# Kernel optimization log

Measured on AMD Instinct MI355X. Metric: run time of the kernel, lower is better.

## Reference

```python
import jax, jax.numpy as jnp
import numpy as np
from jax import lax

LN_EPS = 1e-5
GRN_EPS = 1e-6


def _convnext_block(x, cw, cb, lng, lnb, w1, b1, gg, gb, w2, b2):
    # x: [B, C, H, W] NCHW; cw: [C, 1, 7, 7] depthwise kernel
    dim = x.shape[1]
    y = lax.conv_general_dilated(
        x, cw, window_strides=(1, 1), padding=[(3, 3), (3, 3)],
        dimension_numbers=('NCHW', 'OIHW', 'NCHW'), feature_group_count=dim)
    y = y + cb[None, :, None, None]
    y = y.transpose(0, 2, 3, 1)  # NHWC
    # LayerNorm over channels
    mu = y.mean(-1, keepdims=True)
    var = ((y - mu) ** 2).mean(-1, keepdims=True)
    y = (y - mu) * lax.rsqrt(var + LN_EPS) * lng + lnb
    # pointwise expand
    y = y @ w1 + b1
    y = jax.nn.gelu(y, approximate=False)
    # Global Response Normalization
    gx = jnp.sqrt(jnp.sum(y * y, axis=(1, 2), keepdims=True))  # [B,1,1,C']
    nx = gx / (gx.mean(-1, keepdims=True) + GRN_EPS)
    y = gg * (y * nx) + gb + y
    # pointwise project
    y = y @ w2 + b2
    return y.transpose(0, 3, 1, 2) + x


def _stack_blocks(x, cw, cb, lng, lnb, w1, b1, gg, gb, w2, b2):
    for i in range(cw.shape[0]):
        x = _convnext_block(x, cw[i], cb[i], lng[i], lnb[i], w1[i], b1[i],
                            gg[i], gb[i], w2[i], b2[i])
    return x


def setup_inputs() -> dict:
    key = jax.random.key(0)
    B, C, H, W = 8, 256, 64, 64
    K = 1024
    INTER = 4 * C
    DEPTH = 2
    ks = jax.random.split(key, 8)
    x = jax.random.normal(ks[0], (B, C, H, W), jnp.float32)
    codebook = jax.random.uniform(ks[1], (K, C), jnp.float32, -1.0 / K, 1.0 / K)

    def make_params(k):
        k1, k2, k3 = jax.random.split(k, 3)
        return dict(
            conv_w=0.02 * jax.random.normal(k1, (DEPTH, C, 1, 7, 7), jnp.float32),
            conv_b=jnp.zeros((DEPTH, C), jnp.float32),
            ln_g=jnp.ones((DEPTH, C), jnp.float32),
            ln_b=jnp.zeros((DEPTH, C), jnp.float32),
            fc1_w=0.02 * jax.random.normal(k2, (DEPTH, C, INTER), jnp.float32),
            fc1_b=jnp.zeros((DEPTH, INTER), jnp.float32),
            grn_g=jnp.zeros((DEPTH, INTER), jnp.float32),
            grn_b=jnp.zeros((DEPTH, INTER), jnp.float32),
            fc2_w=0.02 * jax.random.normal(k3, (DEPTH, INTER, C), jnp.float32),
            fc2_b=jnp.zeros((DEPTH, C), jnp.float32),
        )

    enc = make_params(ks[2])
    dec = make_params(ks[3])
    out = {'x': x, 'codebook': codebook}
    for name, p in (('enc', enc), ('dec', dec)):
        for k2, v in p.items():
            out[f'{name}_{k2}'] = v
    return out


def reference(x, codebook,
              enc_conv_w, enc_conv_b, enc_ln_g, enc_ln_b, enc_fc1_w, enc_fc1_b,
              enc_grn_g, enc_grn_b, enc_fc2_w, enc_fc2_b,
              dec_conv_w, dec_conv_b, dec_ln_g, dec_ln_b, dec_fc1_w, dec_fc1_b,
              dec_grn_g, dec_grn_b, dec_fc2_w, dec_fc2_b):
    B, C, H, W = x.shape
    inputs = _stack_blocks(x, enc_conv_w, enc_conv_b, enc_ln_g, enc_ln_b,
                           enc_fc1_w, enc_fc1_b, enc_grn_g, enc_grn_b,
                           enc_fc2_w, enc_fc2_b)
    inputs = inputs.transpose(0, 2, 3, 1)  # [B,H,W,C]
    flat = inputs.reshape(-1, C)  # [N, C]
    # squared Euclidean distances (argmin invariant to sqrt)
    d2 = (jnp.sum(flat * flat, axis=1, keepdims=True)
          - 2.0 * (flat @ codebook.T)
          + jnp.sum(codebook * codebook, axis=1)[None, :])  # [N, K]
    encoding_indices = jnp.argmin(d2, axis=1)  # [N]
    quantized = codebook[encoding_indices].reshape(inputs.shape)  # [B,H,W,C]
    matched_indices = encoding_indices.reshape(B, H, W)
    # straight-through estimator
    quantized = lax.stop_gradient(quantized) + inputs - lax.stop_gradient(inputs)
    quantized = quantized.transpose(0, 3, 1, 2)  # [B,C,H,W]
    decoded = _stack_blocks(quantized, dec_conv_w, dec_conv_b, dec_ln_g, dec_ln_b,
                            dec_fc1_w, dec_fc1_b, dec_grn_g, dec_grn_b,
                            dec_fc2_w, dec_fc2_b)
    return quantized, decoded, matched_indices
```

## Files before the change

### kernel.cpp

```cpp
#include <hip/hip_runtime.h>
#include <math.h>
#include <stdint.h>

typedef unsigned short u16;
typedef unsigned long long u64;
typedef __attribute__((ext_vector_type(8))) short bf16x8;
typedef __attribute__((ext_vector_type(4))) float f32x4;

__device__ __forceinline__ u16 bfhi(float v) {
  unsigned u = __float_as_uint(v);
  u += 0x7FFFu + ((u >> 16) & 1u);
  return (u16)(u >> 16);
}
__device__ __forceinline__ float b2f(u16 h) { return __uint_as_float((unsigned)h << 16); }

__device__ __forceinline__ void gload16(void* lds, const void* g) {
  __builtin_amdgcn_global_load_lds(
      (const __attribute__((address_space(1))) unsigned int*)g,
      (__attribute__((address_space(3))) unsigned int*)lds, 16, 0, 0);
}

__global__ __launch_bounds__(256) void k_conv(const float* __restrict__ in,
                                              const float* __restrict__ cw,
                                              const float* __restrict__ cb,
                                              float* __restrict__ out) {
  const int bx = blockIdx.x;
  const int c = bx & 255;
  __shared__ float patch[70 * 76];
  const int t = threadIdx.x;
  const float* plane = in + (size_t)bx * 4096;
  for (int i = t; i < 1330; i += 256) {
    const int row = i / 19, cf = i - row * 19;
    const int bit = (row >> 2) & 1;
    const int gf = cf - 1 - bit;
    const int h = row - 3;
    float4 v = {0.f, 0.f, 0.f, 0.f};
    if ((unsigned)h < 64u && (unsigned)gf < 16u) v = *(const float4*)(plane + h * 64 + gf * 4);
    *(float4*)(patch + row * 76 + cf * 4) = v;
  }
  const float* wp = cw + c * 49;
  float wt[49];
#pragma unroll
  for (int i = 0; i < 49; ++i) wt[i] = wp[i];
  const float bias = cb[c];
  __syncthreads();
  const int j = t & 7, i = t >> 3;
  const int w0 = j * 8, h0 = i * 2;
  float acc[2][8];
#pragma unroll
  for (int dr = 0; dr < 2; ++dr)
#pragma unroll
    for (int ww = 0; ww < 8; ++ww) acc[dr][ww] = bias;
#pragma unroll
  for (int r = 0; r < 8; ++r) {
    const int prow = h0 + r;
    const int bit = (prow >> 2) & 1;
    const float* base = patch + prow * 76 + w0 + 4 * bit;
    float win[16];
#pragma unroll
    for (int q = 0; q < 4; ++q) {
      const float4 v = *(const float4*)(base + q * 4);
      win[q * 4 + 0] = v.x; win[q * 4 + 1] = v.y;
      win[q * 4 + 2] = v.z; win[q * 4 + 3] = v.w;
    }
#pragma unroll
    for (int dr = 0; dr < 2; ++dr) {
      const int kh = r - dr;
      if (kh >= 0 && kh < 7) {
#pragma unroll
        for (int kw = 0; kw < 7; ++kw) {
          const float wv = wt[kh * 7 + kw];
#pragma unroll
          for (int ww = 0; ww < 8; ++ww)
            acc[dr][ww] = fmaf(win[ww + kw + 1], wv, acc[dr][ww]);
        }
      }
    }
  }
  float* op = out + (size_t)bx * 4096;
#pragma unroll
  for (int dr = 0; dr < 2; ++dr) {
    const int hh = h0 + dr;
    float4 o1, o2;
    o1.x = acc[dr][0]; o1.y = acc[dr][1]; o1.z = acc[dr][2]; o1.w = acc[dr][3];
    o2.x = acc[dr][4]; o2.y = acc[dr][5]; o2.z = acc[dr][6]; o2.w = acc[dr][7];
    *(float4*)(op + hh * 64 + w0) = o1;
    *(float4*)(op + hh * 64 + w0 + 4) = o2;
  }
}

__global__ __launch_bounds__(256) void k_lnT(const float* __restrict__ src,
                                             const float* __restrict__ g,
                                             const float* __restrict__ bt,
                                             u16* __restrict__ Rh, u16* __restrict__ Rl,
                                             const int wlo) {
  __shared__ float T[256 * 33];
  __shared__ float red[8 * 32];
  __shared__ float gs[256], bs[256];
  const int t = threadIdx.x;
  const int n0 = blockIdx.x * 32;
  const int b = n0 >> 12, pl = n0 & 4095;
  gs[t] = g[t];
  bs[t] = bt[t];
  const int m = t & 7, h = t >> 3;
  const float* sp = src + (((size_t)(b * 256)) << 12) + pl + m * 4;
#pragma unroll
  for (int it = 0; it < 8; ++it) {
    const int c = it * 32 + h;
    const float4 v = *(const float4*)(sp + ((size_t)c << 12));
    *(float4*)(T + c * 33 + m * 4) = v;
  }
  __syncthreads();
  const int p = t & 31, qq = t >> 5;
  float s = 0.f;
#pragma unroll
  for (int jj = 0; jj < 32; ++jj) s += T[(qq * 32 + jj) * 33 + p];
  red[qq * 32 + p] = s;
  __syncthreads();
  float tot = 0.f;
#pragma unroll
  for (int k = 0; k < 8; ++k) tot += red[k * 32 + p];
  const float mu = tot * (1.0f / 256.0f);
  __syncthreads();
  float s2 = 0.f;
#pragma unroll
  for (int jj = 0; jj < 32; ++jj) {
    const float d = T[(qq * 32 + jj) * 33 + p] - mu;
    s2 = fmaf(d, d, s2);
  }
  red[qq * 32 + p] = s2;
  __syncthreads();
  float tot2 = 0.f;
#pragma unroll
  for (int k = 0; k < 8; ++k) tot2 += red[k * 32 + p];
  const float rs = 1.0f / sqrtf(tot2 * (1.0f / 256.0f) + 1e-5f);
#pragma unroll
  for (int jj = 0; jj < 32; ++jj) {
    const int c = qq * 32 + jj;
    const float y = (T[c * 33 + p] - mu) * rs * gs[c] + bs[c];
    const u16 hh = bfhi(y);
    const u16 ll = bfhi(y - b2f(hh));
    ((unsigned*)T)[c * 33 + p] = ((unsigned)hh << 16) | ll;
  }
  __syncthreads();
  const int w = t >> 6, l = t & 63;
  const unsigned* Tu = (const unsigned*)T;
#pragma unroll
  for (int r = 0; r < 4; ++r) {
    const int px = r * 8 + w * 2 + (l >> 5);
    const int c0 = (l & 31) * 8;
    unsigned hp[4], lp[4];
#pragma unroll
    for (int jj = 0; jj < 4; ++jj) {
      const unsigned a = Tu[(c0 + 2 * jj) * 33 + px];
      const unsigned bb = Tu[(c0 + 2 * jj + 1) * 33 + px];
      hp[jj] = (a >> 16) | (bb & 0xffff0000u);
      lp[jj] = (a & 0xffffu) | (bb << 16);
    }
    const size_t base = (size_t)(n0 + px) * 256 + c0;
    *(uint4*)(Rh + base) = make_uint4(hp[0], hp[1], hp[2], hp[3]);
    if (wlo) *(uint4*)(Rl + base) = make_uint4(lp[0], lp[1], lp[2], lp[3]);
  }
}

template <int KD, int SPLIT, int EPI, int NCT>
__global__ __launch_bounds__(256) void k_gemm(
    const u16* __restrict__ Ah_, const u16* __restrict__ Al_,
    const u16* __restrict__ Bh_, const u16* __restrict__ Bl_,
    const int row0, const long long bstride,
    const float* __restrict__ pbias,
    u16* __restrict__ poh, u16* __restrict__ pol,
    float* __restrict__ pxout, const float* __restrict__ pxin,
    float* __restrict__ pgx2, u64* __restrict__ pmin) {
  constexpr int BUF_B = (SPLIT ? 4 : 2) * 8192;
  constexpr int NBUF = SPLIT ? 1 : 2;
  constexpr int STAGE_B = NBUF * BUF_B;
  constexpr int TRANS_B = (EPI == 1) ? 64 * 129 * 4 : 0;
  constexpr int SMEM_B = STAGE_B > TRANS_B ? STAGE_B : TRANS_B;
  constexpr int NS = KD / 32;
  __shared__ __align__(16) char smem[SMEM_B];

  const int t = threadIdx.x;
  const int w = t >> 6, l = t & 63;
  const int quad = l >> 4, lm = l & 15;
  const int wr = (w & 1) * 64, wc = (w >> 1) * 64;
  const int id = blockIdx.x + gridDim.x * blockIdx.y;
  constexpr int L = (NCT == 8) ? 3 : 1;
  const int colt = (id >> 3) & (NCT - 1);
  const int rowt = (id & 7) + ((id >> (3 + L)) << 3);
  const int nblk0 = rowt * 128;
  const int bglob = (row0 + nblk0) >> 12;

  const u16* Agh = Ah_ + (size_t)nblk0 * KD;
  const u16* Agl = SPLIT ? (Al_ + (size_t)nblk0 * KD) : Ah_;
  const u16* Bgh = Bh_ + (size_t)bglob * (size_t)bstride + (size_t)(colt * 128) * KD;
  const u16* Bgl = SPLIT ? (Bl_ + (size_t)bglob * (size_t)bstride + (size_t)(colt * 128) * KD) : Bh_;

  f32x4 acc[4][4];
  const f32x4 zz = {0.f, 0.f, 0.f, 0.f};
#pragma unroll
  for (int i = 0; i < 4; ++i)
#pragma unroll
    for (int j = 0; j < 4; ++j) acc[i][j] = zz;

  auto stage32 = [&](char* Sp, const u16* Gp, int ks) {
#pragma unroll
    for (int ii = 0; ii < 2; ++ii) {
      const int o = ii * 4096 + t * 16;
      const int row = o >> 6;
      const int lc = ((o >> 4) & 3) ^ ((row >> 1) & 3);
      gload16(Sp + o, Gp + (size_t)row * KD + ks * 32 + lc * 8);
    }
  };
  auto stage_all = [&](int b, int ks) {
    char* base = smem + (size_t)b * BUF_B;
    stage32(base, Agh, ks);
    stage32(base + 8192, Bgh, ks);
    if constexpr (SPLIT) {
      stage32(base + 16384, Agl, ks);
      stage32(base + 24576, Bgl, ks);
    }
  };
  auto frag_at = [&](const u16* S, int rc) -> bf16x8 {
    const int sw = ((rc >> 1) & 3) ^ quad;
    return *(const bf16x8*)(S + rc * 32 + (sw << 3));
  };

  if constexpr (SPLIT) {
#pragma unroll 1
    for (int ks = 0; ks < NS; ++ks) {
      if (ks) __syncthreads();
      stage_all(0, ks);
      __syncthreads();
      const u16* base = (const u16*)smem;
      bf16x8 ah[4], bh[4], al[4], bl[4];
#pragma unroll
      for (int i = 0; i < 4; ++i) {
        ah[i] = frag_at(base, wr + i * 16 + lm);
        bh[i] = frag_at(base + 4096, wc + i * 16 + lm);
      }
#pragma unroll
      for (int i = 0; i < 4; ++i) {
        al[i] = frag_at(base + 8192, wr + i * 16 + lm);
        bl[i] = frag_at(base + 12288, wc + i * 16 + lm);
      }
#pragma unroll
      for (int i = 0; i < 4; ++i)
#pragma unroll
        for (int j = 0; j < 4; ++j)
          acc[i][j] = __builtin_amdgcn_mfma_f32_16x16x32_bf16(ah[i], bh[j], acc[i][j], 0, 0, 0);
#pragma unroll
      for (int i = 0; i < 4; ++i)
#pragma unroll
        for (int j = 0; j < 4; ++j)
          acc[i][j] = __builtin_amdgcn_mfma_f32_16x16x32_bf16(al[i], bh[j], acc[i][j], 0, 0, 0);
#pragma unroll
      for (int i = 0; i < 4; ++i)
#pragma unroll
        for (int j = 0; j < 4; ++j)
          acc[i][j] = __builtin_amdgcn_mfma_f32_16x16x32_bf16(ah[i], bl[j], acc[i][j], 0, 0, 0);
    }
  } else {
    stage_all(0, 0);
    __syncthreads();
#pragma unroll 1
    for (int ks = 0; ks < NS; ++ks) {
      const u16* base = (const u16*)(smem + (size_t)(ks & 1) * BUF_B);
      bf16x8 ah[4], bh[4];
#pragma unroll
      for (int i = 0; i < 4; ++i) {
        ah[i] = frag_at(base, wr + i * 16 + lm);
        bh[i] = frag_at(base + 4096, wc + i * 16 + lm);
      }
      if (ks + 1 < NS) stage_all((ks + 1) & 1, ks + 1);
      __builtin_amdgcn_sched_barrier(0);
#pragma unroll
      for (int i = 0; i < 4; ++i)
#pragma unroll
        for (int j = 0; j < 4; ++j)
          acc[i][j] = __builtin_amdgcn_mfma_f32_16x16x32_bf16(ah[i], bh[j], acc[i][j], 0, 0, 0);
      __syncthreads();
    }
  }

  if constexpr (EPI == 0) {
    float csum[4] = {0.f, 0.f, 0.f, 0.f};
    float bv[4];
#pragma unroll
    for (int j = 0; j < 4; ++j) bv[j] = pbias[colt * 128 + wc + j * 16 + lm];
#pragma unroll
    for (int i = 0; i < 4; ++i) {
#pragma unroll
      for (int r = 0; r < 4; ++r) {
        const int row = nblk0 + wr + i * 16 + quad * 4 + r;
#pragma unroll
        for (int j = 0; j < 4; ++j) {
          const int col = colt * 128 + wc + j * 16 + lm;
          const float x = acc[i][j][r] + bv[j];
          const float gl = 0.5f * x * (1.0f + erff(x * 0.70710678118654752f));
          csum[j] = fmaf(gl, gl, csum[j]);
          const size_t idx = (size_t)row * 1024 + col;
          const u16 h = bfhi(gl);
          poh[idx] = h;
          if constexpr (SPLIT) pol[idx] = bfhi(gl - b2f(h));
        }
      }
    }
#pragma unroll
    for (int j = 0; j < 4; ++j) {
      float cs = csum[j];
      cs += __shfl_xor(cs, 16);
      cs += __shfl_xor(cs, 32);
      if (quad == 0)
        unsafeAtomicAdd(&pgx2[bglob * 1024 + colt * 128 + wc + j * 16 + lm], cs);
    }
  } else if constexpr (EPI == 1) {
    float* T = (float*)smem;
    const int pg0 = (row0 + nblk0) & 4095;
    const int bb = (row0 + nblk0) >> 12;
#pragma unroll 1
    for (int h = 0; h < 2; ++h) {
      __syncthreads();
      if ((w >> 1) == h) {
#pragma unroll
        for (int i = 0; i < 4; ++i) {
          const int row = wr + i * 16 + quad * 4;
#pragma unroll
          for (int j = 0; j < 4; ++j) {
            const int cl = j * 16 + lm;
#pragma unroll
            for (int r = 0; r < 4; ++r) T[cl * 129 + row + r] = acc[i][j][r];
          }
        }
      }
      __syncthreads();
      const int lp = (l & 31) * 4;
      const int ch2 = l >> 5;
#pragma unroll
      for (int step = 0; step < 8; ++step) {
        const int cl = w * 16 + step * 2 + ch2;
        const int cg = colt * 128 + h * 64 + cl;
        float4 tv = *(float4*)&T[cl * 129 + lp];
        const float bv2 = pbias[cg];
        const size_t nchw = (((size_t)(bb * 256 + cg)) << 12) + pg0 + lp;
        const float4 xv = *(const float4*)(pxin + nchw);
        float4 z;
        z.x = tv.x + bv2 + xv.x;
        z.y = tv.y + bv2 + xv.y;
        z.z = tv.z + bv2 + xv.z;
        z.w = tv.w + bv2 + xv.w;
        if (pxout) *(float4*)(pxout + nchw) = z;
        if (poh) *(float4*)&T[cl * 129 + lp] = z;
      }
      if (poh) {
        __syncthreads();
        const int cl3 = t & 63;
        const int cg3 = colt * 128 + h * 64 + cl3;
        const int r0 = (t >> 6) * 32;
#pragma unroll
        for (int n = 0; n < 32; ++n) {
          const float z = T[cl3 * 129 + r0 + n];
          const size_t idx = (size_t)(nblk0 + r0 + n) * 256 + cg3;
          const u16 hh = bfhi(z);
          poh[idx] = hh;
          pol[idx] = bfhi(z - b2f(hh));
        }
      }
    }
  } else {
#pragma unroll
    for (int i = 0; i < 4; ++i) {
#pragma unroll
      for (int r = 0; r < 4; ++r) {
        const int nloc = nblk0 + wr + i * 16 + quad * 4 + r;
        const float tnv = pxin[nloc];
        u64 best = ~0ULL;
#pragma unroll
        for (int j = 0; j < 4; ++j) {
          const int code = colt * 128 + wc + j * 16 + lm;
          const float d = __fadd_rn(__fsub_rn(tnv, __fmul_rn(2.0f, acc[i][j][r])), pbias[code]);
          const u64 pk = (((u64)__float_as_uint(d)) << 32) | (unsigned)code;
          best = pk < best ? pk : best;
        }
#pragma unroll
        for (int off = 1; off < 16; off <<= 1) {
          unsigned lo32 = (unsigned)best, hi32 = (unsigned)(best >> 32);
          lo32 = __shfl_xor(lo32, off);
          hi32 = __shfl_xor(hi32, off);
          const u64 o2 = (((u64)hi32) << 32) | lo32;
          best = o2 < best ? o2 : best;
        }
        if (lm == 0) atomicMin(pmin + nloc, best);
      }
    }
  }
}

__global__ __launch_bounds__(256) void k_rownorm(const u16* __restrict__ Eh,
                                                 const u16* __restrict__ El,
                                                 float* __restrict__ tn) {
  const int t = threadIdx.x;
  const int r = t >> 2, p = t & 3;
  const int n = blockIdx.x * 64 + r;
  const u16* ph = Eh + (size_t)n * 256 + p * 64;
  const u16* pl = El + (size_t)n * 256 + p * 64;
  float s = 0.f;
#pragma unroll
  for (int j = 0; j < 8; ++j) {
    const uint4 hv = *(const uint4*)(ph + j * 8);
    const uint4 lv = *(const uint4*)(pl + j * 8);
    const unsigned hu[4] = {hv.x, hv.y, hv.z, hv.w};
    const unsigned lu[4] = {lv.x, lv.y, lv.z, lv.w};
#pragma unroll
    for (int q = 0; q < 4; ++q) {
      const float v0 = b2f((u16)(hu[q] & 0xffff)) + b2f((u16)(lu[q] & 0xffff));
      const float v1 = b2f((u16)(hu[q] >> 16)) + b2f((u16)(lu[q] >> 16));
      s = fmaf(v0, v0, s);
      s = fmaf(v1, v1, s);
    }
  }
  s += __shfl_xor(s, 1);
  s += __shfl_xor(s, 2);
  if (p == 0) tn[n] = s;
}

__global__ __launch_bounds__(256) void k_grn_scale(const float* __restrict__ GX2,
                                                   const float* __restrict__ gg,
                                                   float* __restrict__ S, int b0) {
  const int b = b0 + blockIdx.x, t = threadIdx.x;
  const float* gxb = GX2 + (size_t)b * 1024;
  float gx[4];
  float s = 0.f;
#pragma unroll
  for (int i = 0; i < 4; ++i) {
    gx[i] = sqrtf(gxb[t + i * 256]);
    s += gx[i];
  }
  const int w = t >> 6, l = t & 63;
#pragma unroll
  for (int o = 32; o > 0; o >>= 1) s += __shfl_down(s, o);
  __shared__ float red[4];
  __shared__ float bc;
  if (l == 0) red[w] = s;
  __syncthreads();
  if (t == 0) bc = 1.0f / ((red[0] + red[1] + red[2] + red[3]) * (1.0f / 1024.0f) + 1e-6f);
  __syncthreads();
  const float inv = bc;
#pragma unroll
  for (int i = 0; i < 4; ++i)
    S[(size_t)b * 1024 + t + i * 256] = fmaf(gg[t + i * 256], gx[i] * inv, 1.0f);
}

__global__ __launch_bounds__(256) void k_w2prep(const float* __restrict__ W2,
                                                const float* __restrict__ S, int b0,
                                                u16* __restrict__ Wh, u16* __restrict__ Wl) {
  const int bx = blockIdx.x;
  const int b = b0 + (bx >> 8), n = bx & 255;
  const int t = threadIdx.x;
#pragma unroll
  for (int j = 0; j < 4; ++j) {
    const int k = t + j * 256;
    const float v = W2[(size_t)k * 256 + n] * S[(size_t)b * 1024 + k];
    const size_t idx = ((size_t)(b * 256 + n)) * 1024 + k;
    const u16 h = bfhi(v);
    Wh[idx] = h;
    Wl[idx] = bfhi(v - b2f(h));
  }
}

__global__ __launch_bounds__(256) void k_bias2(const float* __restrict__ W2,
                                               const float* __restrict__ gb,
                                               const float* __restrict__ b2,
                                               float* __restrict__ out) {
  const int c = blockIdx.x, t = threadIdx.x;
  float acc = 0.f;
#pragma unroll
  for (int j = 0; j < 4; ++j) {
    const int k = t + j * 256;
    acc = fmaf(gb[k], W2[(size_t)k * 256 + c], acc);
  }
  const int w = t >> 6, l = t & 63;
#pragma unroll
  for (int o = 32; o > 0; o >>= 1) acc += __shfl_down(acc, o);
  __shared__ float red[4];
  if (l == 0) red[w] = acc;
  __syncthreads();
  if (t == 0) out[c] = red[0] + red[1] + red[2] + red[3] + b2[c];
}

__global__ __launch_bounds__(256) void k_wt(const float* __restrict__ W1,
                                            u16* __restrict__ Wh, u16* __restrict__ Wl) {
  const int bx = blockIdx.x;
  const int d = bx >> 10, n = bx & 1023;
  const int k = threadIdx.x;
  const float v = W1[(size_t)d * 262144 + (size_t)k * 1024 + n];
  const size_t idx = (size_t)bx * 256 + k;
  const u16 h = bfhi(v);
  Wh[idx] = h;
  Wl[idx] = bfhi(v - b2f(h));
}

__global__ __launch_bounds__(256) void k_csplit(const float* __restrict__ C,
                                                u16* __restrict__ Ch, u16* __restrict__ Cl) {
  const size_t i = (size_t)blockIdx.x * 256 + threadIdx.x;
  const float v = C[i];
  const u16 h = bfhi(v);
  Ch[i] = h;
  Cl[i] = bfhi(v - b2f(h));
}

__device__ __forceinline__ float np_pairwise_sq_256(const float* p) {
  float half[2];
#pragma unroll
  for (int hh = 0; hh < 2; ++hh) {
    float r[8];
#pragma unroll
    for (int j = 0; j < 8; ++j) {
      const float v = p[hh * 128 + j];
      r[j] = __fmul_rn(v, v);
    }
    for (int i = 8; i < 128; i += 8) {
#pragma unroll
      for (int j = 0; j < 8; ++j) {
        const float v = p[hh * 128 + i + j];
        r[j] = __fadd_rn(r[j], __fmul_rn(v, v));
      }
    }
    half[hh] = __fadd_rn(__fadd_rn(__fadd_rn(r[0], r[1]), __fadd_rn(r[2], r[3])),
                         __fadd_rn(__fadd_rn(r[4], r[5]), __fadd_rn(r[6], r[7])));
  }
  return __fadd_rn(half[0], half[1]);
}

__global__ __launch_bounds__(256) void k_c2(const float* __restrict__ cbk, float* __restrict__ c2) {
  const int k = blockIdx.x * 256 + threadIdx.x;
  c2[k] = np_pairwise_sq_256(cbk + (size_t)k * 256);
}

__global__ __launch_bounds__(256) void k_idx(const u64* __restrict__ pk, float* __restrict__ outI) {
  const int n = blockIdx.x * 256 + threadIdx.x;
  outI[n] = (float)(unsigned)(pk[n] & 0xffffffffULL);
}

__global__ __launch_bounds__(256) void k_gather(const u64* __restrict__ pk,
                                                const float* __restrict__ cbk,
                                                float* __restrict__ outq) {
  const int t = threadIdx.x;
  const int p0 = blockIdx.x * 64;
  const int b = p0 >> 12, pl = (p0 & 4095) + (t & 63);
  const int cg = t >> 6;
  const int n = p0 + (t & 63);
  const int k = (int)(unsigned)(pk[n] & 0xffffffffULL);
  const float* crow = cbk + (size_t)k * 256 + cg * 64;
  float* ob = outq + (((size_t)(b * 256 + cg * 64)) << 12) + pl;
#pragma unroll 1
  for (int j = 0; j < 16; ++j) {
    const float4 cv = *(const float4*)(crow + j * 4);
    ob[((size_t)(j * 4 + 0)) << 12] = cv.x;
    ob[((size_t)(j * 4 + 1)) << 12] = cv.y;
    ob[((size_t)(j * 4 + 2)) << 12] = cv.z;
    ob[((size_t)(j * 4 + 3)) << 12] = cv.w;
  }
}

extern "C" void kernel_launch(void* const* d_in, const int* in_sizes, int n_in,
                              void* d_out, int out_size, void* d_ws, size_t ws_size,
                              hipStream_t stream) {
  const float* x = (const float*)d_in[0];
  const float* cbk = (const float*)d_in[1];
  const float* Pe[10];
  const float* Pd[10];
  for (int i = 0; i < 10; ++i) Pe[i] = (const float*)d_in[2 + i];
  for (int i = 0; i < 10; ++i) Pd[i] = (const float*)d_in[12 + i];

  float* ws = (float*)d_ws;
  size_t o = 0;
  auto alloc = [&](size_t nf) {
    float* p = ws + o;
    o += (nf + 63) & ~(size_t)63;
    return p;
  };
  float* P1 = alloc(8388608);
  u16* Rh = (u16*)alloc(4194304);
  u16* Rl = (u16*)alloc(4194304);
  u16* W1th_e = (u16*)alloc(262144);
  u16* W1tl_e = (u16*)alloc(262144);
  u16* W1th_d = (u16*)alloc(262144);
  u16* W1tl_d = (u16*)alloc(262144);
  u16* W2sh = (u16*)alloc(1048576);
  u16* W2sl = (u16*)alloc(1048576);
  u16* Ch = (u16*)alloc(131072);
  u16* Cl = (u16*)alloc(131072);
  float* C2v = alloc(1024);
  float* GX2 = alloc(8192);
  float* Sv = alloc(8192);
  float* bias2v = alloc(256);
  float* tn = alloc(32768);
  u64* pk = (u64*)alloc(65536);
  const size_t fixedf = o;
  const size_t availf = (ws_size / 4 > fixedf) ? ws_size / 4 - fixedf : 0;
  int chunkB = (int)(availf / 4194304);
  if (chunkB > 8) chunkB = 8;
  if (chunkB < 1) chunkB = 1;
  float* Cv = ws + o;
  u16* Mh = (u16*)(ws + o);
  u16* Ml = (u16*)(ws + o + (size_t)chunkB * 2097152);

  float* outQ = (float*)d_out;
  float* outD = outQ + 8388608;
  float* outI = outD + 8388608;

  auto run_enc = [&](const float* xin, float* xout, u16* Eh, u16* El,
                     const float* const* pp, int d) {
    k_conv<<<2048, 256, 0, stream>>>(xin, pp[0] + (size_t)d * 256 * 49, pp[1] + d * 256, Cv);
    k_lnT<<<1024, 256, 0, stream>>>(Cv, pp[2] + d * 256, pp[3] + d * 256, Rh, Rl, 1);
    k_bias2<<<256, 256, 0, stream>>>(pp[8] + (size_t)d * 262144, pp[7] + d * 1024,
                                     pp[9] + d * 256, bias2v);
    hipMemsetAsync(GX2, 0, 8192 * 4, stream);
    for (int b0 = 0; b0 < 8; b0 += chunkB) {
      const int nb = (8 - b0 < chunkB) ? 8 - b0 : chunkB;
      k_gemm<256, 1, 0, 8><<<dim3(8, nb * 32), 256, 0, stream>>>(
          Rh + (size_t)b0 * 4096 * 256, Rl + (size_t)b0 * 4096 * 256,
          W1th_e + (size_t)d * 262144, W1tl_e + (size_t)d * 262144,
          b0 * 4096, 0, Pe[5] + d * 1024, Mh, Ml, nullptr, nullptr, GX2, nullptr);
      k_grn_scale<<<nb, 256, 0, stream>>>(GX2, pp[6] + d * 1024, Sv, b0);
      k_w2prep<<<nb * 256, 256, 0, stream>>>(pp[8] + (size_t)d * 262144, Sv, b0, W2sh, W2sl);
      k_gemm<1024, 1, 1, 2><<<dim3(2, nb * 32), 256, 0, stream>>>(
          Mh, Ml, W2sh, W2sl, b0 * 4096, 262144LL, bias2v,
          Eh ? Eh + (size_t)b0 * 4096 * 256 : (u16*)nullptr,
          El ? El + (size_t)b0 * 4096 * 256 : (u16*)nullptr,
          xout, xin, nullptr, nullptr);
    }
  };

  auto run_dec = [&](const float* xin, float* xout, const float* const* pp, int d) {
    k_conv<<<2048, 256, 0, stream>>>(xin, pp[0] + (size_t)d * 256 * 49, pp[1] + d * 256, Cv);
    k_lnT<<<1024, 256, 0, stream>>>(Cv, pp[2] + d * 256, pp[3] + d * 256, Rh, Rl, 0);
    k_bias2<<<256, 256, 0, stream>>>(pp[8] + (size_t)d * 262144, pp[7] + d * 1024,
                                     pp[9] + d * 256, bias2v);
    hipMemsetAsync(GX2, 0, 8192 * 4, stream);
    for (int b0 = 0; b0 < 8; b0 += chunkB) {
      const int nb = (8 - b0 < chunkB) ? 8 - b0 : chunkB;
      k_gemm<256, 0, 0, 8><<<dim3(8, nb * 32), 256, 0, stream>>>(
          Rh + (size_t)b0 * 4096 * 256, nullptr,
          W1th_d + (size_t)d * 262144, nullptr,
          b0 * 4096, 0, Pd[5] + d * 1024, Mh, nullptr, nullptr, nullptr, GX2, nullptr);
      k_grn_scale<<<nb, 256, 0, stream>>>(GX2, pp[6] + d * 1024, Sv, b0);
      k_w2prep<<<nb * 256, 256, 0, stream>>>(pp[8] + (size_t)d * 262144, Sv, b0, W2sh, W2sl);
      k_gemm<1024, 0, 1, 2><<<dim3(2, nb * 32), 256, 0, stream>>>(
          Mh, nullptr, W2sh, nullptr, b0 * 4096, 262144LL, bias2v,
          nullptr, nullptr, xout, xin, nullptr, nullptr);
    }
  };

  k_wt<<<2048, 256, 0, stream>>>(Pe[4], W1th_e, W1tl_e);
  k_wt<<<2048, 256, 0, stream>>>(Pd[4], W1th_d, W1tl_d);
  k_csplit<<<1024, 256, 0, stream>>>(cbk, Ch, Cl);
  k_c2<<<4, 256, 0, stream>>>(cbk, C2v);

  run_enc(x, P1, nullptr, nullptr, Pe, 0);
  run_enc(P1, nullptr, Rh, Rl, Pe, 1);

  k_rownorm<<<512, 256, 0, stream>>>(Rh, Rl, tn);
  hipMemsetAsync(pk, 0xFF, 32768 * 8, stream);
  k_gemm<256, 1, 2, 8><<<dim3(8, 256), 256, 0, stream>>>(Rh, Rl, Ch, Cl, 0, 0,
                                                         C2v, nullptr, nullptr, nullptr,
                                                         tn, nullptr, pk);
  k_idx<<<128, 256, 0, stream>>>(pk, outI);
  k_gather<<<512, 256, 0, stream>>>(pk, cbk, outQ);

  run_dec(outQ, P1, Pd, 0);
  run_dec(P1, outD, Pd, 1);
}
```

Baseline: 890.2 us.

## Pre-swizzle B operands into MFMA fragment order and load directly to registers

Weight and codebook prep kernels now write the B matrices in per-wave MFMA fragment order, so the GEMM loads B fragments straight from global memory into registers. Only A is staged through LDS, which halves the shared-memory staging footprint and the LDS traffic for B. The GELU and transpose epilogues also pack four bf16 values per store instead of writing scalar u16. In exchange, B loads are no longer double-buffered through LDS and their global-load latency has to be hidden inside the loop, with B reuse across waves relying on cache.

```diff
diff --git a/kernel.cpp b/kernel.cpp
--- a/kernel.cpp
+++ b/kernel.cpp
@@ -172,9 +172,9 @@
     u16* __restrict__ poh, u16* __restrict__ pol,
     float* __restrict__ pxout, const float* __restrict__ pxin,
     float* __restrict__ pgx2, u64* __restrict__ pmin) {
-  constexpr int BUF_B = (SPLIT ? 4 : 2) * 8192;
+  constexpr int ABUF_B = (SPLIT ? 2 : 1) * 8192;
   constexpr int NBUF = SPLIT ? 1 : 2;
-  constexpr int STAGE_B = NBUF * BUF_B;
+  constexpr int STAGE_B = NBUF * ABUF_B;
   constexpr int TRANS_B = (EPI == 1) ? 64 * 129 * 4 : 0;
   constexpr int SMEM_B = STAGE_B > TRANS_B ? STAGE_B : TRANS_B;
   constexpr int NS = KD / 32;
@@ -193,8 +193,10 @@
 
   const u16* Agh = Ah_ + (size_t)nblk0 * KD;
   const u16* Agl = SPLIT ? (Al_ + (size_t)nblk0 * KD) : Ah_;
-  const u16* Bgh = Bh_ + (size_t)bglob * (size_t)bstride + (size_t)(colt * 128) * KD;
-  const u16* Bgl = SPLIT ? (Bl_ + (size_t)bglob * (size_t)bstride + (size_t)(colt * 128) * KD) : Bh_;
+  const size_t bfo = (size_t)bglob * (size_t)bstride +
+                     (size_t)((colt * 2 + (w >> 1)) * NS * 4) * 512 + (size_t)l * 8;
+  const u16* Bfh = Bh_ + bfo;
+  const u16* Bfl = SPLIT ? (Bl_ + bfo) : Bfh;
 
   f32x4 acc[4][4];
   const f32x4 zz = {0.f, 0.f, 0.f, 0.f};
@@ -212,15 +214,6 @@
       gload16(Sp + o, Gp + (size_t)row * KD + ks * 32 + lc * 8);
     }
   };
-  auto stage_all = [&](int b, int ks) {
-    char* base = smem + (size_t)b * BUF_B;
-    stage32(base, Agh, ks);
-    stage32(base + 8192, Bgh, ks);
-    if constexpr (SPLIT) {
-      stage32(base + 16384, Agl, ks);
-      stage32(base + 24576, Bgl, ks);
-    }
-  };
   auto frag_at = [&](const u16* S, int rc) -> bf16x8 {
     const int sw = ((rc >> 1) & 3) ^ quad;
     return *(const bf16x8*)(S + rc * 32 + (sw << 3));
@@ -230,19 +223,20 @@
 #pragma unroll 1
     for (int ks = 0; ks < NS; ++ks) {
       if (ks) __syncthreads();
-      stage_all(0, ks);
+      stage32(smem, Agh, ks);
+      stage32(smem + 8192, Agl, ks);
+      bf16x8 bh[4], bl[4];
+#pragma unroll
+      for (int i = 0; i < 4; ++i) bh[i] = *(const bf16x8*)(Bfh + (ks * 4 + i) * 512);
+#pragma unroll
+      for (int i = 0; i < 4; ++i) bl[i] = *(const bf16x8*)(Bfl + (ks * 4 + i) * 512);
       __syncthreads();
       const u16* base = (const u16*)smem;
-      bf16x8 ah[4], bh[4], al[4], bl[4];
+      bf16x8 ah[4], al[4];
 #pragma unroll
       for (int i = 0; i < 4; ++i) {
         ah[i] = frag_at(base, wr + i * 16 + lm);
-        bh[i] = frag_at(base + 4096, wc + i * 16 + lm);
-      }
-#pragma unroll
-      for (int i = 0; i < 4; ++i) {
-        al[i] = frag_at(base + 8192, wr + i * 16 + lm);
-        bl[i] = frag_at(base + 12288, wc + i * 16 + lm);
+        al[i] = frag_at(base + 4096, wr + i * 16 + lm);
       }
 #pragma unroll
       for (int i = 0; i < 4; ++i)
@@ -261,18 +255,17 @@
           acc[i][j] = __builtin_amdgcn_mfma_f32_16x16x32_bf16(ah[i], bl[j], acc[i][j], 0, 0, 0);
     }
   } else {
-    stage_all(0, 0);
+    stage32(smem, Agh, 0);
     __syncthreads();
 #pragma unroll 1
     for (int ks = 0; ks < NS; ++ks) {
-      const u16* base = (const u16*)(smem + (size_t)(ks & 1) * BUF_B);
+      const u16* base = (const u16*)(smem + (size_t)(ks & 1) * ABUF_B);
       bf16x8 ah[4], bh[4];
 #pragma unroll
-      for (int i = 0; i < 4; ++i) {
-        ah[i] = frag_at(base, wr + i * 16 + lm);
-        bh[i] = frag_at(base + 4096, wc + i * 16 + lm);
-      }
-      if (ks + 1 < NS) stage_all((ks + 1) & 1, ks + 1);
+      for (int i = 0; i < 4; ++i) bh[i] = *(const bf16x8*)(Bfh + (ks * 4 + i) * 512);
+#pragma unroll
+      for (int i = 0; i < 4; ++i) ah[i] = frag_at(base, wr + i * 16 + lm);
+      if (ks + 1 < NS) stage32(smem + (size_t)((ks + 1) & 1) * ABUF_B, Agh, ks + 1);
       __builtin_amdgcn_sched_barrier(0);
 #pragma unroll
       for (int i = 0; i < 4; ++i)
@@ -293,17 +286,20 @@
 #pragma unroll
       for (int r = 0; r < 4; ++r) {
         const int row = nblk0 + wr + i * 16 + quad * 4 + r;
+        unsigned hp[4], lp[4];
 #pragma unroll
         for (int j = 0; j < 4; ++j) {
-          const int col = colt * 128 + wc + j * 16 + lm;
           const float x = acc[i][j][r] + bv[j];
           const float gl = 0.5f * x * (1.0f + erff(x * 0.70710678118654752f));
           csum[j] = fmaf(gl, gl, csum[j]);
-          const size_t idx = (size_t)row * 1024 + col;
           const u16 h = bfhi(gl);
-          poh[idx] = h;
-          if constexpr (SPLIT) pol[idx] = bfhi(gl - b2f(h));
+          hp[j] = h;
+          if constexpr (SPLIT) lp[j] = bfhi(gl - b2f(h));
         }
+        const size_t ob = (size_t)row * 1024 + colt * 128 + wc + lm * 4;
+        *(uint2*)(poh + ob) = make_uint2(hp[0] | (hp[1] << 16), hp[2] | (hp[3] << 16));
+        if constexpr (SPLIT)
+          *(uint2*)(pol + ob) = make_uint2(lp[0] | (lp[1] << 16), lp[2] | (lp[3] << 16));
       }
     }
 #pragma unroll
@@ -354,16 +350,23 @@
       }
       if (poh) {
         __syncthreads();
-        const int cl3 = t & 63;
-        const int cg3 = colt * 128 + h * 64 + cl3;
-        const int r0 = (t >> 6) * 32;
-#pragma unroll
-        for (int n = 0; n < 32; ++n) {
-          const float z = T[cl3 * 129 + r0 + n];
-          const size_t idx = (size_t)(nblk0 + r0 + n) * 256 + cg3;
-          const u16 hh = bfhi(z);
-          poh[idx] = hh;
-          pol[idx] = bfhi(z - b2f(hh));
+        const int u = t & 15, c4 = u * 4;
+        const int rg = t >> 4;
+        const int cg4 = colt * 128 + h * 64 + c4;
+#pragma unroll
+        for (int n = 0; n < 8; ++n) {
+          const int row = rg + 16 * n;
+          unsigned hp[4], lp4[4];
+#pragma unroll
+          for (int q = 0; q < 4; ++q) {
+            const float z = T[(c4 + q) * 129 + row];
+            const u16 hh = bfhi(z);
+            hp[q] = hh;
+            lp4[q] = bfhi(z - b2f(hh));
+          }
+          const size_t idx = (size_t)(nblk0 + row) * 256 + cg4;
+          *(uint2*)(poh + idx) = make_uint2(hp[0] | (hp[1] << 16), hp[2] | (hp[3] << 16));
+          *(uint2*)(pol + idx) = make_uint2(lp4[0] | (lp4[1] << 16), lp4[2] | (lp4[3] << 16));
         }
       }
     }
@@ -451,20 +454,26 @@
     S[(size_t)b * 1024 + t + i * 256] = fmaf(gg[t + i * 256], gx[i] * inv, 1.0f);
 }
 
-__global__ __launch_bounds__(256) void k_w2prep(const float* __restrict__ W2,
-                                                const float* __restrict__ S, int b0,
-                                                u16* __restrict__ Wh, u16* __restrict__ Wl) {
+__global__ __launch_bounds__(256) void k_w2prepf(const float* __restrict__ W2,
+                                                 const float* __restrict__ S, int b0,
+                                                 u16* __restrict__ Wh, u16* __restrict__ Wl) {
   const int bx = blockIdx.x;
-  const int b = b0 + (bx >> 8), n = bx & 255;
-  const int t = threadIdx.x;
-#pragma unroll
-  for (int j = 0; j < 4; ++j) {
-    const int k = t + j * 256;
-    const float v = W2[(size_t)k * 256 + n] * S[(size_t)b * 1024 + k];
-    const size_t idx = ((size_t)(b * 256 + n)) * 1024 + k;
+  const int b = b0 + (bx >> 9);
+  const int cid = bx & 511;
+  const int colt = cid >> 8, wcw = (cid >> 7) & 1, ks = (cid >> 2) & 31, j = cid & 3;
+  const int t = threadIdx.x, l = t & 63, e0 = (t >> 6) * 2;
+  const int n = colt * 128 + wcw * 64 + j * 16 + (l & 15);
+  const int kl = ks * 32 + (l >> 4) * 8 + e0;
+  const size_t ob = (size_t)b * 262144 + (size_t)cid * 512 + l * 8 + e0;
+#pragma unroll
+  for (int q = 0; q < 2; ++q) {
+    const int klq = kl + q;
+    const int y = klq & 63;
+    const int ko = (klq & ~63) | ((y & 3) << 4) | (y >> 2);
+    const float v = W2[(size_t)ko * 256 + n] * S[(size_t)b * 1024 + ko];
     const u16 h = bfhi(v);
-    Wh[idx] = h;
-    Wl[idx] = bfhi(v - b2f(h));
+    Wh[ob + q] = h;
+    Wl[ob + q] = bfhi(v - b2f(h));
   }
 }
 
@@ -488,25 +497,40 @@
   if (t == 0) out[c] = red[0] + red[1] + red[2] + red[3] + b2[c];
 }
 
-__global__ __launch_bounds__(256) void k_wt(const float* __restrict__ W1,
-                                            u16* __restrict__ Wh, u16* __restrict__ Wl) {
+__global__ __launch_bounds__(256) void k_wtf(const float* __restrict__ W1,
+                                             u16* __restrict__ Wh, u16* __restrict__ Wl) {
   const int bx = blockIdx.x;
-  const int d = bx >> 10, n = bx & 1023;
-  const int k = threadIdx.x;
-  const float v = W1[(size_t)d * 262144 + (size_t)k * 1024 + n];
-  const size_t idx = (size_t)bx * 256 + k;
-  const u16 h = bfhi(v);
-  Wh[idx] = h;
-  Wl[idx] = bfhi(v - b2f(h));
-}
-
-__global__ __launch_bounds__(256) void k_csplit(const float* __restrict__ C,
-                                                u16* __restrict__ Ch, u16* __restrict__ Cl) {
-  const size_t i = (size_t)blockIdx.x * 256 + threadIdx.x;
-  const float v = C[i];
-  const u16 h = bfhi(v);
-  Ch[i] = h;
-  Cl[i] = bfhi(v - b2f(h));
+  const int d = bx >> 9, cid = bx & 511;
+  const int colt = cid >> 6, wcw = (cid >> 5) & 1, ks = (cid >> 2) & 7, j = cid & 3;
+  const int t = threadIdx.x, l = t & 63, e0 = (t >> 6) * 2;
+  const int n = colt * 128 + wcw * 64 + j * 16 + (l & 15);
+  const int k = ks * 32 + (l >> 4) * 8 + e0;
+  const float* src = W1 + (size_t)d * 262144;
+  const size_t ob = (size_t)bx * 512 + l * 8 + e0;
+#pragma unroll
+  for (int q = 0; q < 2; ++q) {
+    const float v = src[(size_t)(k + q) * 1024 + n];
+    const u16 h = bfhi(v);
+    Wh[ob + q] = h;
+    Wl[ob + q] = bfhi(v - b2f(h));
+  }
+}
+
+__global__ __launch_bounds__(256) void k_csplitf(const float* __restrict__ C,
+                                                 u16* __restrict__ Ch, u16* __restrict__ Cl) {
+  const int cid = blockIdx.x;
+  const int colt = cid >> 6, wcw = (cid >> 5) & 1, ks = (cid >> 2) & 7, j = cid & 3;
+  const int t = threadIdx.x, l = t & 63, e0 = (t >> 6) * 2;
+  const int code = colt * 128 + wcw * 64 + j * 16 + (l & 15);
+  const int ch = ks * 32 + (l >> 4) * 8 + e0;
+  const size_t ob = (size_t)cid * 512 + l * 8 + e0;
+#pragma unroll
+  for (int q = 0; q < 2; ++q) {
+    const float v = C[(size_t)code * 256 + ch + q];
+    const u16 h = bfhi(v);
+    Ch[ob + q] = h;
+    Cl[ob + q] = bfhi(v - b2f(h));
+  }
 }
 
 __device__ __forceinline__ float np_pairwise_sq_256(const float* p) {
@@ -624,7 +648,7 @@
           W1th_e + (size_t)d * 262144, W1tl_e + (size_t)d * 262144,
           b0 * 4096, 0, Pe[5] + d * 1024, Mh, Ml, nullptr, nullptr, GX2, nullptr);
       k_grn_scale<<<nb, 256, 0, stream>>>(GX2, pp[6] + d * 1024, Sv, b0);
-      k_w2prep<<<nb * 256, 256, 0, stream>>>(pp[8] + (size_t)d * 262144, Sv, b0, W2sh, W2sl);
+      k_w2prepf<<<nb * 512, 256, 0, stream>>>(pp[8] + (size_t)d * 262144, Sv, b0, W2sh, W2sl);
       k_gemm<1024, 1, 1, 2><<<dim3(2, nb * 32), 256, 0, stream>>>(
           Mh, Ml, W2sh, W2sl, b0 * 4096, 262144LL, bias2v,
           Eh ? Eh + (size_t)b0 * 4096 * 256 : (u16*)nullptr,
@@ -646,16 +670,16 @@
           W1th_d + (size_t)d * 262144, nullptr,
           b0 * 4096, 0, Pd[5] + d * 1024, Mh, nullptr, nullptr, nullptr, GX2, nullptr);
       k_grn_scale<<<nb, 256, 0, stream>>>(GX2, pp[6] + d * 1024, Sv, b0);
-      k_w2prep<<<nb * 256, 256, 0, stream>>>(pp[8] + (size_t)d * 262144, Sv, b0, W2sh, W2sl);
+      k_w2prepf<<<nb * 512, 256, 0, stream>>>(pp[8] + (size_t)d * 262144, Sv, b0, W2sh, W2sl);
       k_gemm<1024, 0, 1, 2><<<dim3(2, nb * 32), 256, 0, stream>>>(
           Mh, nullptr, W2sh, nullptr, b0 * 4096, 262144LL, bias2v,
           nullptr, nullptr, xout, xin, nullptr, nullptr);
     }
   };
 
-  k_wt<<<2048, 256, 0, stream>>>(Pe[4], W1th_e, W1tl_e);
-  k_wt<<<2048, 256, 0, stream>>>(Pd[4], W1th_d, W1tl_d);
-  k_csplit<<<1024, 256, 0, stream>>>(cbk, Ch, Cl);
+  k_wtf<<<1024, 256, 0, stream>>>(Pe[4], W1th_e, W1tl_e);
+  k_wtf<<<1024, 256, 0, stream>>>(Pd[4], W1th_d, W1tl_d);
+  k_csplitf<<<512, 256, 0, stream>>>(cbk, Ch, Cl);
   k_c2<<<4, 256, 0, stream>>>(cbk, C2v);
 
   run_enc(x, P1, nullptr, nullptr, Pe, 0);
```

Result: faster. 865.9 us (-2.7%).
